# Performance work log

Measured on AMD Instinct MI355X. Metric: run time of the kernel, lower is better.

## Reference

```python
import jax, jax.numpy as jnp
import numpy as np
import math

B, S, D, H, DFF = 4, 1024, 1024, 16, 4096
DH = D // H
ALPHA = 1.0
NEG = -1e20
EPS = 1e-5


def layernorm(x, g, b):
    mu = jnp.mean(x, axis=-1, keepdims=True)
    var = jnp.mean((x - mu) ** 2, axis=-1, keepdims=True)
    return (x - mu) * jax.lax.rsqrt(var + EPS) * g + b


def setup_inputs() -> dict:
    key = jax.random.key(0)
    ks = jax.random.split(key, 16)
    sc = 1.0 / math.sqrt(D)
    inp = {
        "x": jax.random.normal(ks[0], (B, S, D), jnp.float32),
        "mask": jnp.ones((B, 1, S), jnp.float32),
        "Wq": jax.random.normal(ks[1], (D, D), jnp.float32) * sc,
        "Wk": jax.random.normal(ks[2], (D, D), jnp.float32) * sc,
        "Wv": jax.random.normal(ks[3], (D, D), jnp.float32) * sc,
        "ln1_g": jnp.ones((DH,), jnp.float32),
        "ln1_b": jnp.zeros((DH,), jnp.float32),
        "Wo": jax.random.normal(ks[4], (D, D), jnp.float32) * sc,
        "bo": jnp.zeros((D,), jnp.float32),
        "ln2_g": jnp.ones((D,), jnp.float32),
        "ln2_b": jnp.zeros((D,), jnp.float32),
        "Ws": jax.random.normal(ks[5], (D, D), jnp.float32) * sc,
        "Wh": jax.random.normal(ks[6], (D, D), jnp.float32) * sc,
        "b_f": jnp.zeros((D,), jnp.float32),
        "lnfg_g": jnp.ones((D,), jnp.float32),
        "lnfg_b": jnp.zeros((D,), jnp.float32),
        "Wp1": jax.random.normal(ks[7], (DFF, D), jnp.float32) * sc,
        "bp1": jnp.zeros((DFF,), jnp.float32),
        "Wp2": jax.random.normal(ks[8], (D, DFF), jnp.float32) / math.sqrt(DFF),
        "bp2": jnp.zeros((D,), jnp.float32),
        "lnffn_g": jnp.ones((D,), jnp.float32),
        "lnffn_b": jnp.zeros((D,), jnp.float32),
    }
    return inp


def reference(x, mask, Wq, Wk, Wv, ln1_g, ln1_b, Wo, bo, ln2_g, ln2_b,
              Ws, Wh, b_f, lnfg_g, lnfg_b, Wp1, bp1, Wp2, bp2, lnffn_g, lnffn_b):
    b, s, d = x.shape
    # --- masked multi-head attention ---
    q = (x @ Wq.T).reshape(b, s, H, DH)
    k = (x @ Wk.T).reshape(b, s, H, DH)
    v = (x @ Wv.T).reshape(b, s, H, DH)
    q = layernorm(q, ln1_g, ln1_b)
    k = layernorm(k, ln1_g, ln1_b)
    v = layernorm(v, ln1_g, ln1_b)
    energy = jnp.einsum('nqhd,nkhd->nhqk', q, k)  # (B,H,S,S)
    # directional mask: forward pass -> strictly lower triangular allowed (0), else -1e20
    idx = jnp.arange(s)
    allowed = idx[:, None] > idx[None, :]  # tril(diagonal=-1)
    dir_mask = jnp.where(allowed, 0.0, NEG).astype(x.dtype)  # (S,S)
    m = jnp.broadcast_to(mask, (b, H, s))  # (B,H,S)
    pair = m[:, :, :, None] * m[:, :, None, :]  # (B,H,S,S)
    final_mask = pair * dir_mask[None, None]
    dist_mask = -jnp.abs(idx[:, None] - idx[None, :]).astype(x.dtype)  # (S,S)
    pre = energy / math.sqrt(d) + final_mask + ALPHA * dist_mask[None, None]
    attn = jax.nn.softmax(pre, axis=-1)
    # faithful to source einsum 'nhql,nlhd->nlhd' (sums attention over q)
    out = jnp.einsum('nhql,nlhd->nlhd', attn, v)
    out = out.reshape(b, s, d)
    out = out @ Wo.T + bo
    h = layernorm(out, ln2_g, ln2_b)
    # --- fusion gate and norm ---
    s_f = layernorm(x @ Ws.T, lnfg_g, lnfg_b)
    h_f = layernorm(h @ Wh.T, lnfg_g, lnfg_b)
    f = jax.nn.sigmoid(s_f + h_f + b_f)
    g = layernorm(f * s_f + (1.0 - f) * h_f, lnfg_g, lnfg_b)
    # --- position-wise FFN + residual + norm ---
    ff = jax.nn.relu(g @ Wp1.T + bp1) @ Wp2.T + bp2
    return layernorm(ff + g, lnffn_g, lnffn_b)
```

## Files before the change

### kernel.cpp

```cpp
#include <hip/hip_runtime.h>

constexpr int CB   = 4;
constexpr int CS   = 1024;
constexpr int CD   = 1024;
constexpr int CH   = 16;
constexpr int CDFF = 4096;
constexpr int CNT  = CB * CS;

typedef unsigned short ush;
typedef __bf16 bf16_t;
typedef bf16_t bf16x8 __attribute__((ext_vector_type(8)));
typedef float  f32x4  __attribute__((ext_vector_type(4)));

__device__ __forceinline__ ush f2bf(float f) {
    union { float f; unsigned u; } v; v.f = f;
    unsigned u = v.u;
    return (ush)((u + 0x7fffu + ((u >> 16) & 1u)) >> 16);
}
__device__ __forceinline__ float bf2f(ush h) {
    union { unsigned u; float f; } v; v.u = ((unsigned)h) << 16;
    return v.f;
}
__device__ __forceinline__ void ub8(uint4 v, float* d) {
    d[0] = bf2f((ush)v.x); d[1] = bf2f((ush)(v.x >> 16));
    d[2] = bf2f((ush)v.y); d[3] = bf2f((ush)(v.y >> 16));
    d[4] = bf2f((ush)v.z); d[5] = bf2f((ush)(v.z >> 16));
    d[6] = bf2f((ush)v.w); d[7] = bf2f((ush)(v.w >> 16));
}
__device__ __forceinline__ uint4 pb8(const float* d) {
    uint4 v;
    v.x = (unsigned)f2bf(d[0]) | ((unsigned)f2bf(d[1]) << 16);
    v.y = (unsigned)f2bf(d[2]) | ((unsigned)f2bf(d[3]) << 16);
    v.z = (unsigned)f2bf(d[4]) | ((unsigned)f2bf(d[5]) << 16);
    v.w = (unsigned)f2bf(d[6]) | ((unsigned)f2bf(d[7]) << 16);
    return v;
}

__device__ __forceinline__ void gll16(const void* g, void* l) {
    __builtin_amdgcn_global_load_lds((const __attribute__((address_space(1))) void*)g,
                                     (__attribute__((address_space(3))) void*)l,
                                     16, 0, 0);
}

constexpr int Q4 = (CD * CD) / 4;
__global__ __launch_bounds__(256) void k_convert_all(
        const float4* __restrict__ Wq, const float4* __restrict__ Wk,
        const float4* __restrict__ Wv, const float4* __restrict__ Ws,
        const float4* __restrict__ Wo, const float4* __restrict__ Wh,
        const float4* __restrict__ Wp1, const float4* __restrict__ Wp2,
        const float4* __restrict__ x, uint4* __restrict__ arena,
        uint4* __restrict__ xb, float4* __restrict__ wz) {
    int i = blockIdx.x * 256 + threadIdx.x;
    int stride = gridDim.x * 256;
    for (int i2 = i; i2 < (CB * CH * CS) / 4; i2 += stride)
        wz[i2] = (float4){0.f, 0.f, 0.f, 0.f};
    for (; i < 9 * Q4; i += stride) {
        const int F = i * 2;
        const int seg = F >> 18;
        const float4* src; int off;
        if (seg < 6) {
            src = (seg == 0) ? Wq : (seg == 1) ? Wk : (seg == 2) ? Wv
                : (seg == 3) ? Ws : (seg == 4) ? Wo : Wh;
            off = F & (Q4 - 1);
        } else if (seg < 10) { src = Wp1; off = F - 6 * Q4; }
        else if (seg < 14)   { src = Wp2; off = F - 10 * Q4; }
        else                 { src = x;   off = F - 14 * Q4; }
        float4 a = src[off], b = src[off + 1];
        uint4 o;
        o.x = (unsigned)f2bf(a.x) | ((unsigned)f2bf(a.y) << 16);
        o.y = (unsigned)f2bf(a.z) | ((unsigned)f2bf(a.w) << 16);
        o.z = (unsigned)f2bf(b.x) | ((unsigned)f2bf(b.y) << 16);
        o.w = (unsigned)f2bf(b.z) | ((unsigned)f2bf(b.w) << 16);
        if (seg < 14) arena[i] = o;
        else          xb[i - 7 * Q4] = o;
    }
}

template <int EPI>
__global__ __launch_bounds__(512) void k_gemm_p4(
        const ush* __restrict__ A, const ush* __restrict__ Bm,
        ush* __restrict__ Cb,
        const float* __restrict__ bias, const float* __restrict__ bias2,
        ush* __restrict__ out2, ush* __restrict__ out3, ush* __restrict__ sb,
        int N, int K) {
    __shared__ ush sm[4 * 16384];

    const int tid  = threadIdx.x;
    const int wave = tid >> 6, lane = tid & 63;
    const int quad = lane >> 4, r = lane & 15;
    const int wm = wave >> 1, wn = wave & 1;
    const int bm = blockIdx.x, bn = blockIdx.y;
    const int NT = K >> 6;

    const int trow = tid >> 3, tk8 = tid & 7;
    const int kcl  = tk8 ^ (trow & 7);
    const ush* ap = A  + (size_t)(bm * 128 + trow) * K + kcl * 8;
    const ush* bp = Bm + (size_t)(bn * 128 + trow) * K + kcl * 8;

    f32x4 acc[2][4];
#pragma unroll
    for (int i = 0; i < 2; i++)
#pragma unroll
        for (int j = 0; j < 4; j++) acc[i][j] = (f32x4){0.f, 0.f, 0.f, 0.f};

    auto STAGE = [&](int tt) {
        ush* sl = sm + (tt & 3) * 16384;
        const ush* aq = ap + tt * 64;
        const ush* bq = bp + tt * 64;
        gll16(aq,                  sl + tid * 8);
        gll16(aq + (size_t)64 * K, sl + 4096  + tid * 8);
        gll16(bq,                  sl + 8192  + tid * 8);
        gll16(bq + (size_t)64 * K, sl + 12288 + tid * 8);
    };

    STAGE(0); STAGE(1); STAGE(2);
    asm volatile("s_waitcnt vmcnt(8)" ::: "memory");
    __builtin_amdgcn_s_barrier();

    const int rx = r & 7;
    for (int t = 0; t < NT; ++t) {
        if (t + 3 < NT) STAGE(t + 3);
        const ush* sA = sm + (t & 3) * 16384;
        const ush* sB = sA + 8192;
        __builtin_amdgcn_s_setprio(1);
#pragma unroll
        for (int h = 0; h < 2; ++h) {
            const int kx = (((h << 2) | quad) ^ rx) * 8;
            bf16x8 af[2], bfv[4];
#pragma unroll
            for (int i = 0; i < 2; i++)
                af[i] = *(const bf16x8*)(sA + (wm * 32 + i * 16 + r) * 64 + kx);
#pragma unroll
            for (int j = 0; j < 4; j++)
                bfv[j] = *(const bf16x8*)(sB + (wn * 64 + j * 16 + r) * 64 + kx);
#pragma unroll
            for (int i = 0; i < 2; i++)
#pragma unroll
                for (int j = 0; j < 4; j++)
                    acc[i][j] = __builtin_amdgcn_mfma_f32_16x16x32_bf16(af[i], bfv[j], acc[i][j], 0, 0, 0);
        }
        __builtin_amdgcn_s_setprio(0);
        const int rem = NT - 1 - t;
        if (rem >= 3)      asm volatile("s_waitcnt vmcnt(8)" ::: "memory");
        else if (rem == 2) asm volatile("s_waitcnt vmcnt(4)" ::: "memory");
        else if (rem == 1) asm volatile("s_waitcnt vmcnt(0)" ::: "memory");
        if (rem) __builtin_amdgcn_s_barrier();
    }

    __syncthreads();
    constexpr int EPS2 = 136;
    ush* Cs = sm;

    if (EPI == 4 && (bn >> 3) < 3) {
        float g4[4], b4[4];
#pragma unroll
        for (int j = 0; j < 4; j++) { g4[j] = bias[j * 16 + r]; b4[j] = bias2[j * 16 + r]; }
#pragma unroll
        for (int i = 0; i < 2; i++) {
            const int row = wm * 32 + i * 16 + quad * 4;
#pragma unroll
            for (int g = 0; g < 4; g++) {
                float s = 0.f, q = 0.f;
#pragma unroll
                for (int j = 0; j < 4; j++) { float v = acc[i][j][g]; s += v; q += v * v; }
                s += __shfl_xor(s, 1); q += __shfl_xor(q, 1);
                s += __shfl_xor(s, 2); q += __shfl_xor(q, 2);
                s += __shfl_xor(s, 4); q += __shfl_xor(q, 4);
                s += __shfl_xor(s, 8); q += __shfl_xor(q, 8);
                float mu   = s * (1.f / 64.f);
                float rstd = rsqrtf(q * (1.f / 64.f) - mu * mu + 1e-5f);
#pragma unroll
                for (int j = 0; j < 4; j++) {
                    float y = (acc[i][j][g] - mu) * rstd * g4[j] + b4[j];
                    Cs[(row + g) * EPS2 + wn * 64 + j * 16 + r] = f2bf(y);
                }
            }
        }
    } else {
#pragma unroll
        for (int i = 0; i < 2; i++) {
            const int row = wm * 32 + i * 16 + quad * 4;
#pragma unroll
            for (int j = 0; j < 4; j++) {
                const int col = wn * 64 + j * 16 + r;
                float bv = (EPI == 3) ? bias[bn * 128 + col] : 0.f;
#pragma unroll
                for (int g = 0; g < 4; g++) {
                    float v = acc[i][j][g] + bv;
                    if (EPI == 3) v = fmaxf(v, 0.f);
                    Cs[(row + g) * EPS2 + col] = f2bf(v);
                }
            }
        }
    }
    __syncthreads();

    ush* dst = Cb; int colbase = bn * 128, Nn = N;
    if (EPI == 4) {
        Nn = 1024;
        const int quarter = bn >> 3;
        colbase = (bn & 7) * 128;
        dst = (quarter == 0) ? Cb : (quarter == 1) ? out2 : (quarter == 2) ? out3 : sb;
    }
#pragma unroll
    for (int p = 0; p < 4; p++) {
        const int rr = p * 32 + (tid >> 4);
        const int cc = (tid & 15) * 8;
        uint4 vv = *(const uint4*)&Cs[rr * EPS2 + cc];
        *(uint4*)&dst[(size_t)(bm * 128 + rr) * Nn + colbase + cc] = vv;
    }
}

__global__ __launch_bounds__(256) void k_attn(const ush* __restrict__ qb,
                                              const ush* __restrict__ kb,
                                              const float* __restrict__ mask,
                                              float* __restrict__ wcol) {
    __shared__ ush   Qs[64][72];
    __shared__ ush   Ks[64][72];
    __shared__ float colpart[4][64];

    const int tid  = threadIdx.x;
    const int wave = tid >> 6, lane = tid & 63;
    const int quad = lane >> 4, r = lane & 15;
    const int bh = blockIdx.x, bi = bh >> 4, hi = bh & 15;
    const int q0 = blockIdx.y * 64;

    {
        int row = tid >> 2, seg = (tid & 3) * 16;
        const ush* src = qb + ((size_t)(bi * CS + q0 + row) * CD + hi * 64 + seg);
        *(uint4*)&Qs[row][seg]     = *(const uint4*)src;
        *(uint4*)&Qs[row][seg + 8] = *(const uint4*)(src + 8);
    }
    __syncthreads();
    bf16x8 af0 = *(const bf16x8*)&Qs[wave * 16 + r][quad * 8];
    bf16x8 af1 = *(const bf16x8*)&Qs[wave * 16 + r][32 + quad * 8];

    float mq[4];
#pragma unroll
    for (int g = 0; g < 4; g++) mq[g] = mask[bi * CS + q0 + wave * 16 + quad * 4 + g];

    const int t0 = (q0 >= 128) ? 0 : ((q0 >= 64) ? 1 : 2);
    float pr[3][4][4];
    float s_loc[4] = {0.f, 0.f, 0.f, 0.f};

    for (int t = t0; t < 3; t++) {
        const int l0 = q0 - 128 + t * 64;
        __syncthreads();
        {
            int row = tid >> 2, seg = (tid & 3) * 16;
            const ush* src = kb + ((size_t)(bi * CS + l0 + row) * CD + hi * 64 + seg);
            *(uint4*)&Ks[row][seg]     = *(const uint4*)src;
            *(uint4*)&Ks[row][seg + 8] = *(const uint4*)(src + 8);
        }
        __syncthreads();
#pragma unroll
        for (int jt = 0; jt < 4; jt++) {
            bf16x8 bf0 = *(const bf16x8*)&Ks[jt * 16 + r][quad * 8];
            bf16x8 bf1 = *(const bf16x8*)&Ks[jt * 16 + r][32 + quad * 8];
            f32x4 sc = (f32x4){0.f, 0.f, 0.f, 0.f};
            sc = __builtin_amdgcn_mfma_f32_16x16x32_bf16(af0, bf0, sc, 0, 0, 0);
            sc = __builtin_amdgcn_mfma_f32_16x16x32_bf16(af1, bf1, sc, 0, 0, 0);
            const int l = l0 + jt * 16 + r;
            const float ml = mask[bi * CS + l];
#pragma unroll
            for (int g = 0; g < 4; g++) {
                const int qg = q0 + wave * 16 + quad * 4 + g;
                float e  = sc[g] * 0.03125f;
                float mv = (qg > l) ? 0.f : mq[g] * ml * (-1e20f);
                float p  = __expf(e + mv - fabsf((float)(qg - l)) - 8.f);
                pr[t][jt][g] = p;
                s_loc[g] += p;
            }
        }
    }

    float rs[4];
#pragma unroll
    for (int g = 0; g < 4; g++) {
        float s = s_loc[g];
        s += __shfl_xor(s, 1); s += __shfl_xor(s, 2);
        s += __shfl_xor(s, 4); s += __shfl_xor(s, 8);
        rs[g] = (s > 0.f) ? 1.f / s : 0.f;
    }

    for (int t = t0; t < 3; t++) {
        const int l0 = q0 - 128 + t * 64;
#pragma unroll
        for (int jt = 0; jt < 4; jt++) {
            float csum = 0.f;
#pragma unroll
            for (int g = 0; g < 4; g++) csum += pr[t][jt][g] * rs[g];
            csum += __shfl_xor(csum, 16);
            csum += __shfl_xor(csum, 32);
            if (quad == 0) colpart[wave][jt * 16 + r] = csum;
        }
        __syncthreads();
        if (tid < 64) {
            float v = colpart[0][tid] + colpart[1][tid] + colpart[2][tid] + colpart[3][tid];
            atomicAdd(&wcol[(size_t)bh * CS + l0 + tid], v);
        }
        __syncthreads();
    }
}

__global__ __launch_bounds__(256) void k_scale_v(const ush* __restrict__ vb,
                                                 const float* __restrict__ wcol,
                                                 ush* __restrict__ out) {
    const int g = blockIdx.x * 256 + threadIdx.x;
    const int token = g >> 7;
    const int cg = g & 127;
    const int c0 = cg * 8, h = cg >> 3;
    const int l = token & (CS - 1), b = token >> 10;
    const float w = wcol[(size_t)(b * CH + h) * CS + l] + (1.f / 1024.f);
    float d[8];
    ub8(*(const uint4*)&vb[(size_t)token * CD + c0], d);
#pragma unroll
    for (int j = 0; j < 8; j++) d[j] *= w;
    *(uint4*)&out[(size_t)token * CD + c0] = pb8(d);
}

__device__ __forceinline__ void stats128(float s, float q, float* red,
                                         int wave, int lane, float& mu, float& rstd) {
#pragma unroll
    for (int off = 32; off >= 1; off >>= 1) {
        s += __shfl_xor(s, off);
        q += __shfl_xor(q, off);
    }
    if (lane == 0) { red[wave] = s; red[2 + wave] = q; }
    __syncthreads();
    s = red[0] + red[1];
    q = red[2] + red[3];
    mu = s * (1.f / 1024.f);
    rstd = rsqrtf(q * (1.f / 1024.f) - mu * mu + 1e-5f);
    __syncthreads();
}

template <int MODE>
__global__ __launch_bounds__(128) void k_ln_row(const ush* __restrict__ b0,
                                                const ush* __restrict__ b1,
                                                const ush* __restrict__ b2,
                                                const float* __restrict__ badd,
                                                const float* __restrict__ gam,
                                                const float* __restrict__ bet,
                                                float* __restrict__ outf,
                                                ush* __restrict__ outb) {
    __shared__ float red[4];
    const int tid = threadIdx.x, wave = tid >> 6, lane = tid & 63;
    const size_t base = (size_t)blockIdx.x * CD;
    const int c0 = tid * 8;
    float t[8], sr[8], tmp[8], gv[8], bv[8];
    float s = 0.f, q = 0.f, mu, rstd;

    *(float4*)&gv[0] = *(const float4*)&gam[c0];
    *(float4*)&gv[4] = *(const float4*)&gam[c0 + 4];
    *(float4*)&bv[0] = *(const float4*)&bet[c0];
    *(float4*)&bv[4] = *(const float4*)&bet[c0 + 4];

    if (MODE == 2) {
        float av[8];
        *(float4*)&av[0] = *(const float4*)&badd[c0];
        *(float4*)&av[4] = *(const float4*)&badd[c0 + 4];
        ub8(*(const uint4*)&b0[base + c0], sr);
        ub8(*(const uint4*)&b1[base + c0], t);
#pragma unroll
        for (int j = 0; j < 8; j++) { s += sr[j]; q += sr[j] * sr[j]; }
        stats128(s, q, red, wave, lane, mu, rstd);
#pragma unroll
        for (int j = 0; j < 8; j++) sr[j] = (sr[j] - mu) * rstd * gv[j] + bv[j];
        s = 0.f; q = 0.f;
#pragma unroll
        for (int j = 0; j < 8; j++) { s += t[j]; q += t[j] * t[j]; }
        stats128(s, q, red, wave, lane, mu, rstd);
#pragma unroll
        for (int j = 0; j < 8; j++) {
            float hf = (t[j] - mu) * rstd * gv[j] + bv[j];
            float f  = 1.f / (1.f + __expf(-(sr[j] + hf + av[j])));
            t[j] = f * sr[j] + (1.f - f) * hf;
        }
    } else {
        float av[8];
        *(float4*)&av[0] = *(const float4*)&badd[c0];
        *(float4*)&av[4] = *(const float4*)&badd[c0 + 4];
        ub8(*(const uint4*)&b0[base + c0], t);
#pragma unroll
        for (int j = 0; j < 8; j++) t[j] += av[j];
        if (MODE == 3) {
            ub8(*(const uint4*)&b2[base + c0], tmp);
#pragma unroll
            for (int j = 0; j < 8; j++) t[j] += tmp[j];
        }
    }

    s = 0.f; q = 0.f;
#pragma unroll
    for (int j = 0; j < 8; j++) { s += t[j]; q += t[j] * t[j]; }
    stats128(s, q, red, wave, lane, mu, rstd);

    float y[8];
#pragma unroll
    for (int j = 0; j < 8; j++) y[j] = (t[j] - mu) * rstd * gv[j] + bv[j];
    if (MODE == 3) {
        *(float4*)&outf[base + c0]     = *(float4*)&y[0];
        *(float4*)&outf[base + c0 + 4] = *(float4*)&y[4];
    } else {
        *(uint4*)&outb[base + c0] = pb8(y);
    }
}

extern "C" void kernel_launch(void* const* d_in, const int* in_sizes, int n_in,
                              void* d_out, int out_size, void* d_ws, size_t ws_size,
                              hipStream_t stream) {
    const float* x    = (const float*)d_in[0];
    const float* mask = (const float*)d_in[1];
    const float* Wq   = (const float*)d_in[2];
    const float* Wk   = (const float*)d_in[3];
    const float* Wv   = (const float*)d_in[4];
    const float* ln1g = (const float*)d_in[5];
    const float* ln1b = (const float*)d_in[6];
    const float* Wo   = (const float*)d_in[7];
    const float* bo   = (const float*)d_in[8];
    const float* ln2g = (const float*)d_in[9];
    const float* ln2b = (const float*)d_in[10];
    const float* Ws   = (const float*)d_in[11];
    const float* Wh   = (const float*)d_in[12];
    const float* bf_  = (const float*)d_in[13];
    const float* lnfgg = (const float*)d_in[14];
    const float* lnfgb = (const float*)d_in[15];
    const float* Wp1  = (const float*)d_in[16];
    const float* bp1  = (const float*)d_in[17];
    const float* Wp2  = (const float*)d_in[18];
    const float* bp2  = (const float*)d_in[19];
    const float* lnffg = (const float*)d_in[20];
    const float* lnffb = (const float*)d_in[21];
    float* out = (float*)d_out;

    char* p = (char*)d_ws;
    auto alloc = [&](size_t bytes) -> char* {
        char* r = p;
        p += (bytes + 255) & ~(size_t)255;
        return r;
    };
    ush*   arena = (ush*)alloc((size_t)14 * CD * CD * 2);
    ush*   Wob   = arena + (size_t)4 * CD * CD;
    ush*   Whb   = arena + (size_t)5 * CD * CD;
    ush*   Wp1b  = arena + (size_t)6 * CD * CD;
    ush*   Wp2b  = arena + (size_t)10 * CD * CD;
    ush*   xb    = (ush*)alloc((size_t)CNT * CD * 2);
    ush*   klnb  = (ush*)alloc((size_t)CNT * CD * 2);
    ush*   vb    = (ush*)alloc((size_t)CNT * CD * 2);
    ush*   qlnb  = (ush*)alloc((size_t)CNT * CD * 2);
    ush*   gb    = (ush*)alloc((size_t)CNT * CD * 2);
    ush*   P     = (ush*)alloc((size_t)2 * CNT * CD * 2);
    ush*   P1    = P + (size_t)CNT * CD;
    ush*   ff1b  = (ush*)alloc((size_t)CNT * CDFF * 2);
    float* wcol  = (float*)alloc((size_t)CB * CH * CS * 4);
    ush*   sbuf  = ff1b;
    ush*   attb  = qlnb;
    ush*   hb    = klnb;

    dim3 blk(256);
    dim3 gblk(512);

    k_convert_all<<<dim3(4608), blk, 0, stream>>>(
        (const float4*)Wq, (const float4*)Wk, (const float4*)Wv, (const float4*)Ws,
        (const float4*)Wo, (const float4*)Wh, (const float4*)Wp1, (const float4*)Wp2,
        (const float4*)x, (uint4*)arena, (uint4*)xb, (float4*)wcol);

    k_gemm_p4<4><<<dim3(32, 32), gblk, 0, stream>>>(
        xb, arena, qlnb, ln1g, ln1b, klnb, vb, sbuf, 4096, CD);

    k_attn<<<dim3(CB * CH, CS / 64), blk, 0, stream>>>(qlnb, klnb, mask, wcol);
    k_scale_v<<<dim3(CNT * CD / 8 / 256), blk, 0, stream>>>(vb, wcol, attb);

    k_gemm_p4<0><<<dim3(32, 8), gblk, 0, stream>>>(
        attb, Wob, P, nullptr, nullptr, nullptr, nullptr, nullptr, CD, CD);
    k_ln_row<0><<<dim3(CNT), dim3(128), 0, stream>>>(P, nullptr, nullptr, bo, ln2g, ln2b, nullptr, hb);

    k_gemm_p4<0><<<dim3(32, 8), gblk, 0, stream>>>(
        hb, Whb, P1, nullptr, nullptr, nullptr, nullptr, nullptr, CD, CD);
    k_ln_row<2><<<dim3(CNT), dim3(128), 0, stream>>>(sbuf, P1, nullptr, bf_, lnfgg, lnfgb, nullptr, gb);

    k_gemm_p4<3><<<dim3(32, 32), gblk, 0, stream>>>(
        gb, Wp1b, ff1b, bp1, nullptr, nullptr, nullptr, nullptr, CDFF, CD);
    k_gemm_p4<0><<<dim3(32, 8), gblk, 0, stream>>>(
        ff1b, Wp2b, P, nullptr, nullptr, nullptr, nullptr, nullptr, CD, CDFF);
    k_ln_row<3><<<dim3(CNT), dim3(128), 0, stream>>>(P, nullptr, gb, bp2, lnffg, lnffb, out, nullptr);

    (void)in_sizes; (void)n_in; (void)out_size; (void)ws_size;
}
```

Baseline: 368.5 us.

## Enlarge GEMM tile to 256x128 with 3-stage interleaved pipeline and split-K

The GEMM kernel changes from a 128x128 to a 256x128 block tile with a 4x4 MFMA accumulator grid per wave. It uses a 3-slot shared-memory ring whose A and B prefetches are interleaved between two half-compute phases. The N=1024 GEMMs use split-K of 2, writing two bf16 partials that the following layernorm kernels add together. This aims to raise arithmetic intensity and fill the GPU on the small-N GEMMs. The costs are higher register pressure, extra partial-buffer traffic, and bf16 rounding of each partial before the sum.

Result: no change. 367.7 us (-0.2%).

```diff
diff --git a/kernel.cpp b/kernel.cpp
--- a/kernel.cpp
+++ b/kernel.cpp
@@ -76,78 +76,123 @@
     }
 }
 
-template <int EPI>
-__global__ __launch_bounds__(512) void k_gemm_p4(
+template <int EPI, int SPLITK>
+__global__ __launch_bounds__(512, 2) void k_gemm3(
         const ush* __restrict__ A, const ush* __restrict__ Bm,
         ush* __restrict__ Cb,
         const float* __restrict__ bias, const float* __restrict__ bias2,
         ush* __restrict__ out2, ush* __restrict__ out3, ush* __restrict__ sb,
         int N, int K) {
-    __shared__ ush sm[4 * 16384];
+    __shared__ ush sm[3 * 24576];
 
     const int tid  = threadIdx.x;
     const int wave = tid >> 6, lane = tid & 63;
     const int quad = lane >> 4, r = lane & 15;
     const int wm = wave >> 1, wn = wave & 1;
     const int bm = blockIdx.x, bn = blockIdx.y;
-    const int NT = K >> 6;
-
-    const int trow = tid >> 3, tk8 = tid & 7;
-    const int kcl  = tk8 ^ (trow & 7);
-    const ush* ap = A  + (size_t)(bm * 128 + trow) * K + kcl * 8;
-    const ush* bp = Bm + (size_t)(bn * 128 + trow) * K + kcl * 8;
-
-    f32x4 acc[2][4];
-#pragma unroll
-    for (int i = 0; i < 2; i++)
+    const int kcnt  = K / SPLITK;
+    const int kbase = blockIdx.z * kcnt;
+    const int NT = kcnt >> 6;
+    ush* dst0 = Cb;
+    if (SPLITK > 1) dst0 += (size_t)blockIdx.z * (size_t)gridDim.x * 256 * N;
+
+    const int trow = tid >> 3;
+    const int kcl  = (tid & 7) ^ (trow & 7);
+    const ush* ap = A  + (size_t)(bm * 256 + trow) * K + kbase + kcl * 8;
+    const ush* bp = Bm + (size_t)(bn * 128 + trow) * K + kbase + kcl * 8;
+
+    f32x4 acc[4][4];
+#pragma unroll
+    for (int i = 0; i < 4; i++)
 #pragma unroll
         for (int j = 0; j < 4; j++) acc[i][j] = (f32x4){0.f, 0.f, 0.f, 0.f};
 
-    auto STAGE = [&](int tt) {
-        ush* sl = sm + (tt & 3) * 16384;
-        const ush* aq = ap + tt * 64;
-        const ush* bq = bp + tt * 64;
-        gll16(aq,                  sl + tid * 8);
-        gll16(aq + (size_t)64 * K, sl + 4096  + tid * 8);
-        gll16(bq,                  sl + 8192  + tid * 8);
-        gll16(bq + (size_t)64 * K, sl + 12288 + tid * 8);
+    auto STAGE_A = [&](int slot, int tt) {
+        ush* d = sm + slot * 24576 + tid * 8;
+        const ush* s0 = ap + tt * 64;
+        gll16(s0,                    d);
+        gll16(s0 + (size_t)64  * K,  d + 4096);
+        gll16(s0 + (size_t)128 * K,  d + 8192);
+        gll16(s0 + (size_t)192 * K,  d + 12288);
     };
-
-    STAGE(0); STAGE(1); STAGE(2);
-    asm volatile("s_waitcnt vmcnt(8)" ::: "memory");
+    auto STAGE_B = [&](int slot, int tt) {
+        ush* d = sm + slot * 24576 + 16384 + tid * 8;
+        const ush* s0 = bp + tt * 64;
+        gll16(s0,                   d);
+        gll16(s0 + (size_t)64 * K,  d + 4096);
+    };
+
+    STAGE_A(0, 0); STAGE_B(0, 0);
+    STAGE_A(1, 1); STAGE_B(1, 1);
+    asm volatile("s_waitcnt vmcnt(6)" ::: "memory");
     __builtin_amdgcn_s_barrier();
 
-    const int rx = r & 7;
+    int cs = 0, ss = 2;
     for (int t = 0; t < NT; ++t) {
-        if (t + 3 < NT) STAGE(t + 3);
-        const ush* sA = sm + (t & 3) * 16384;
-        const ush* sB = sA + 8192;
+        const ush* sA = sm + cs * 24576;
+        const ush* sB = sA + 16384;
+        const bool st = (t + 2) < NT;
+
+        bf16x8 bq[4][2], a0[2][2];
+#pragma unroll
+        for (int j = 0; j < 4; j++)
+#pragma unroll
+            for (int h = 0; h < 2; h++) {
+                const int row = wn * 64 + j * 16 + r;
+                bq[j][h] = *(const bf16x8*)(sB + row * 64 + ((((h << 2) | quad) ^ (row & 7)) << 3));
+            }
+#pragma unroll
+        for (int i = 0; i < 2; i++)
+#pragma unroll
+            for (int h = 0; h < 2; h++) {
+                const int row = wm * 64 + i * 16 + r;
+                a0[i][h] = *(const bf16x8*)(sA + row * 64 + ((((h << 2) | quad) ^ (row & 7)) << 3));
+            }
+        if (st) STAGE_A(ss, t + 2);
+        __builtin_amdgcn_s_barrier();
+        asm volatile("s_waitcnt lgkmcnt(0)" ::: "memory");
         __builtin_amdgcn_s_setprio(1);
 #pragma unroll
-        for (int h = 0; h < 2; ++h) {
-            const int kx = (((h << 2) | quad) ^ rx) * 8;
-            bf16x8 af[2], bfv[4];
-#pragma unroll
-            for (int i = 0; i < 2; i++)
-                af[i] = *(const bf16x8*)(sA + (wm * 32 + i * 16 + r) * 64 + kx);
+        for (int i = 0; i < 2; i++)
 #pragma unroll
             for (int j = 0; j < 4; j++)
-                bfv[j] = *(const bf16x8*)(sB + (wn * 64 + j * 16 + r) * 64 + kx);
-#pragma unroll
-            for (int i = 0; i < 2; i++)
-#pragma unroll
-                for (int j = 0; j < 4; j++)
-                    acc[i][j] = __builtin_amdgcn_mfma_f32_16x16x32_bf16(af[i], bfv[j], acc[i][j], 0, 0, 0);
-        }
+#pragma unroll
+                for (int h = 0; h < 2; h++)
+                    acc[i][j] = __builtin_amdgcn_mfma_f32_16x16x32_bf16(a0[i][h], bq[j][h], acc[i][j], 0, 0, 0);
         __builtin_amdgcn_s_setprio(0);
-        const int rem = NT - 1 - t;
-        if (rem >= 3)      asm volatile("s_waitcnt vmcnt(8)" ::: "memory");
-        else if (rem == 2) asm volatile("s_waitcnt vmcnt(4)" ::: "memory");
-        else if (rem == 1) asm volatile("s_waitcnt vmcnt(0)" ::: "memory");
-        if (rem) __builtin_amdgcn_s_barrier();
-    }
-
+        __builtin_amdgcn_s_barrier();
+
+        bf16x8 a1[2][2];
+#pragma unroll
+        for (int i = 0; i < 2; i++)
+#pragma unroll
+            for (int h = 0; h < 2; h++) {
+                const int row = wm * 64 + (i + 2) * 16 + r;
+                a1[i][h] = *(const bf16x8*)(sA + row * 64 + ((((h << 2) | quad) ^ (row & 7)) << 3));
+            }
+        if (st) STAGE_B(ss, t + 2);
+        __builtin_amdgcn_s_barrier();
+        asm volatile("s_waitcnt lgkmcnt(0)" ::: "memory");
+        __builtin_amdgcn_s_setprio(1);
+#pragma unroll
+        for (int i = 0; i < 2; i++)
+#pragma unroll
+            for (int j = 0; j < 4; j++)
+#pragma unroll
+                for (int h = 0; h < 2; h++)
+                    acc[i + 2][j] = __builtin_amdgcn_mfma_f32_16x16x32_bf16(a1[i][h], bq[j][h], acc[i + 2][j], 0, 0, 0);
+        __builtin_amdgcn_s_setprio(0);
+
+        if (t < NT - 1) {
+            if (st) asm volatile("s_waitcnt vmcnt(6)" ::: "memory");
+            else    asm volatile("s_waitcnt vmcnt(0)" ::: "memory");
+            __builtin_amdgcn_s_barrier();
+        }
+        cs = (cs == 2) ? 0 : cs + 1;
+        ss = (ss == 2) ? 0 : ss + 1;
+    }
     __syncthreads();
+
     constexpr int EPS2 = 136;
     ush* Cs = sm;
 
@@ -156,8 +201,8 @@
 #pragma unroll
         for (int j = 0; j < 4; j++) { g4[j] = bias[j * 16 + r]; b4[j] = bias2[j * 16 + r]; }
 #pragma unroll
-        for (int i = 0; i < 2; i++) {
-            const int row = wm * 32 + i * 16 + quad * 4;
+        for (int i = 0; i < 4; i++) {
+            const int row = wm * 64 + i * 16 + quad * 4;
 #pragma unroll
             for (int g = 0; g < 4; g++) {
                 float s = 0.f, q = 0.f;
@@ -178,8 +223,8 @@
         }
     } else {
 #pragma unroll
-        for (int i = 0; i < 2; i++) {
-            const int row = wm * 32 + i * 16 + quad * 4;
+        for (int i = 0; i < 4; i++) {
+            const int row = wm * 64 + i * 16 + quad * 4;
 #pragma unroll
             for (int j = 0; j < 4; j++) {
                 const int col = wn * 64 + j * 16 + r;
@@ -195,7 +240,7 @@
     }
     __syncthreads();
 
-    ush* dst = Cb; int colbase = bn * 128, Nn = N;
+    ush* dst = dst0; int colbase = bn * 128, Nn = N;
     if (EPI == 4) {
         Nn = 1024;
         const int quarter = bn >> 3;
@@ -203,11 +248,11 @@
         dst = (quarter == 0) ? Cb : (quarter == 1) ? out2 : (quarter == 2) ? out3 : sb;
     }
 #pragma unroll
-    for (int p = 0; p < 4; p++) {
+    for (int p = 0; p < 8; p++) {
         const int rr = p * 32 + (tid >> 4);
         const int cc = (tid & 15) * 8;
         uint4 vv = *(const uint4*)&Cs[rr * EPS2 + cc];
-        *(uint4*)&dst[(size_t)(bm * 128 + rr) * Nn + colbase + cc] = vv;
+        *(uint4*)&dst[(size_t)(bm * 256 + rr) * Nn + colbase + cc] = vv;
     }
 }
 
@@ -362,6 +407,9 @@
         *(float4*)&av[4] = *(const float4*)&badd[c0 + 4];
         ub8(*(const uint4*)&b0[base + c0], sr);
         ub8(*(const uint4*)&b1[base + c0], t);
+        ub8(*(const uint4*)&b2[base + c0], tmp);
+#pragma unroll
+        for (int j = 0; j < 8; j++) t[j] += tmp[j];
 #pragma unroll
         for (int j = 0; j < 8; j++) { s += sr[j]; q += sr[j] * sr[j]; }
         stats128(s, q, red, wave, lane, mu, rstd);
@@ -382,8 +430,9 @@
         *(float4*)&av[0] = *(const float4*)&badd[c0];
         *(float4*)&av[4] = *(const float4*)&badd[c0 + 4];
         ub8(*(const uint4*)&b0[base + c0], t);
-#pragma unroll
-        for (int j = 0; j < 8; j++) t[j] += av[j];
+        ub8(*(const uint4*)&b1[base + c0], tmp);
+#pragma unroll
+        for (int j = 0; j < 8; j++) t[j] += tmp[j] + av[j];
         if (MODE == 3) {
             ub8(*(const uint4*)&b2[base + c0], tmp);
 #pragma unroll
@@ -466,25 +515,25 @@
         (const float4*)Wo, (const float4*)Wh, (const float4*)Wp1, (const float4*)Wp2,
         (const float4*)x, (uint4*)arena, (uint4*)xb, (float4*)wcol);
 
-    k_gemm_p4<4><<<dim3(32, 32), gblk, 0, stream>>>(
+    k_gemm3<4, 1><<<dim3(16, 32, 1), gblk, 0, stream>>>(
         xb, arena, qlnb, ln1g, ln1b, klnb, vb, sbuf, 4096, CD);
 
     k_attn<<<dim3(CB * CH, CS / 64), blk, 0, stream>>>(qlnb, klnb, mask, wcol);
     k_scale_v<<<dim3(CNT * CD / 8 / 256), blk, 0, stream>>>(vb, wcol, attb);
 
-    k_gemm_p4<0><<<dim3(32, 8), gblk, 0, stream>>>(
+    k_gemm3<0, 2><<<dim3(16, 8, 2), gblk, 0, stream>>>(
         attb, Wob, P, nullptr, nullptr, nullptr, nullptr, nullptr, CD, CD);
-    k_ln_row<0><<<dim3(CNT), dim3(128), 0, stream>>>(P, nullptr, nullptr, bo, ln2g, ln2b, nullptr, hb);
-
-    k_gemm_p4<0><<<dim3(32, 8), gblk, 0, stream>>>(
-        hb, Whb, P1, nullptr, nullptr, nullptr, nullptr, nullptr, CD, CD);
-    k_ln_row<2><<<dim3(CNT), dim3(128), 0, stream>>>(sbuf, P1, nullptr, bf_, lnfgg, lnfgb, nullptr, gb);
-
-    k_gemm_p4<3><<<dim3(32, 32), gblk, 0, stream>>>(
+    k_ln_row<0><<<dim3(CNT), dim3(128), 0, stream>>>(P, P1, nullptr, bo, ln2g, ln2b, nullptr, hb);
+
+    k_gemm3<0, 2><<<dim3(16, 8, 2), gblk, 0, stream>>>(
+        hb, Whb, P, nullptr, nullptr, nullptr, nullptr, nullptr, CD, CD);
+    k_ln_row<2><<<dim3(CNT), dim3(128), 0, stream>>>(sbuf, P, P1, bf_, lnfgg, lnfgb, nullptr, gb);
+
+    k_gemm3<3, 1><<<dim3(16, 32, 1), gblk, 0, stream>>>(
         gb, Wp1b, ff1b, bp1, nullptr, nullptr, nullptr, nullptr, CDFF, CD);
-    k_gemm_p4<0><<<dim3(32, 8), gblk, 0, stream>>>(
+    k_gemm3<0, 2><<<dim3(16, 8, 2), gblk, 0, stream>>>(
         ff1b, Wp2b, P, nullptr, nullptr, nullptr, nullptr, nullptr, CD, CDFF);
-    k_ln_row<3><<<dim3(CNT), dim3(128), 0, stream>>>(P, nullptr, gb, bp2, lnffg, lnffb, out, nullptr);
+    k_ln_row<3><<<dim3(CNT), dim3(128), 0, stream>>>(P, P1, gb, bp2, lnffg, lnffb, out, nullptr);
 
     (void)in_sizes; (void)n_in; (void)out_size; (void)ws_size;
 }
```
